# Kernel tuning notes

Measured on AMD Instinct MI355X. Metric: run time of the kernel, lower is better.

## Reference

```python
import jax, jax.numpy as jnp
import numpy as np

EPS = 1e-07


def unfold(a, p):
    # torch F.unfold(a, p, padding=(p-1)//2, stride=1): [B,C,H,W] -> [B, C*p*p, H*W]
    B, C, H, W = a.shape
    pad = (p - 1) // 2
    ap = jnp.pad(a, ((0, 0), (0, 0), (pad, pad), (pad, pad)))
    # channel ordering is C-major then (kh, kw), matching torch unfold
    patches = jnp.stack([ap[:, :, i:i + H, j:j + W] for i in range(p) for j in range(p)], axis=2)
    return patches.reshape(B, C * p * p, H * W)


def linear_attn(q, k, x):
    # q:[B,h,l1,d1]  k:[B,h,l2,d1]  x:[B,h,l2,d2]
    l1, d1 = q.shape[-2:]
    l2, d2 = x.shape[-2:]
    kt = jnp.swapaxes(k, -2, -1)  # [B,h,d1,l2]
    if l1 * d1 * l2 + l1 * l2 * d2 <= d2 * l2 * d1 + d2 * d1 * l1:
        s = q @ kt                                        # [B,h,l1,l2]
        s = s / (s.sum(axis=-1, keepdims=True) + EPS)
        return s @ x
    else:
        out = q @ (kt @ x)                                # [B,h,l1,d2]
        denom = q @ kt.sum(axis=-1, keepdims=True) + EPS  # [B,h,l1,1]
        return out / denom


def setup_inputs() -> dict:
    key = jax.random.key(0)
    k1, k2, k3, k4, k5 = jax.random.split(key, 5)
    B, C, H, W = 4, 64, 128, 128
    x = jax.random.normal(k1, (B, C, H, W), dtype=jnp.float32)
    qkv_w = jax.random.normal(k2, (3 * C, C), dtype=jnp.float32) * 0.05
    qkv_b = jax.random.normal(k3, (3 * C,), dtype=jnp.float32) * 0.01
    proj_w = jax.random.normal(k4, (C, C, 3, 3), dtype=jnp.float32) * 0.05
    proj_b = jax.random.normal(k5, (C,), dtype=jnp.float32) * 0.01
    return {"x": x, "qkv_w": qkv_w, "qkv_b": qkv_b, "proj_w": proj_w, "proj_b": proj_b}


def reference(x, qkv_w, qkv_b, proj_w, proj_b):
    numHeads, patchSize = 8, 3
    B, C, H, W = x.shape
    L = H * W
    # 1x1 conv qkv
    qkv = jnp.einsum('bchw,oc->bohw', x, qkv_w) + qkv_b[None, :, None, None]
    q, k, v = qkv[:, :C], qkv[:, C:2 * C], qkv[:, 2 * C:]
    q = jax.nn.relu(q)
    k = jax.nn.relu(k)
    q = unfold(q, patchSize)  # [B, C*p*p, L]
    k = unfold(k, patchSize)
    v = v.reshape(B, C, L)
    d1 = C * patchSize * patchSize
    assert d1 % numHeads == 0  # chosen so replicate-pad branch is skipped
    q = jnp.swapaxes(q.reshape(B, numHeads, d1 // numHeads, L), -1, -2)   # [B,h,L,d1h]
    k = jnp.swapaxes(k.reshape(B, numHeads, d1 // numHeads, L), -1, -2)
    v = jnp.swapaxes(v.reshape(B, numHeads, C // numHeads, L), -1, -2)    # [B,h,L,d2h]
    out = linear_attn(q, k, v)                                            # [B,h,L,d2h]
    out = jnp.swapaxes(out, -1, -2).reshape(B, C, H, W)
    # 3x3 conv proj, padding 1
    out = jax.lax.conv_general_dilated(out, proj_w, window_strides=(1, 1), padding='SAME',
                                       dimension_numbers=('NCHW', 'OIHW', 'NCHW'))
    out = out + proj_b[None, :, None, None]
    return out
```

## Files before the change

### kernel.cpp

```cpp
#include <hip/hip_runtime.h>
#include <hip/hip_fp16.h>

#define LL 16384
#define HH 128
#define WW 128
#define CC 64
#define NH 8
#define EPSF 1e-7f
#define KVCHUNKS 32

typedef __attribute__((ext_vector_type(8))) _Float16 f16x8;
typedef __attribute__((ext_vector_type(4))) float f32x4;
typedef __attribute__((ext_vector_type(8))) unsigned short u16x8;

static __device__ __forceinline__ unsigned short f2h_bits(float v) {
    const _Float16 h = (_Float16)v;
    unsigned short b;
    __builtin_memcpy(&b, &h, 2);
    return b;
}
static __device__ __forceinline__ float h2f_u16(unsigned short s) {
    _Float16 h;
    __builtin_memcpy(&h, &s, 2);
    return (float)h;
}
static __device__ __forceinline__ float h2f_lo(unsigned int u) {
    return h2f_u16((unsigned short)(u & 0xffffu));
}
static __device__ __forceinline__ float h2f_hi(unsigned int u) {
    return h2f_u16((unsigned short)(u >> 16));
}

__global__ void qkv_kernel(const float* __restrict__ x, const float* __restrict__ w,
                           const float* __restrict__ bias,
                           unsigned short* __restrict__ q, unsigned short* __restrict__ k,
                           unsigned short* __restrict__ v) {
    const int pix0 = blockIdx.x * 128;
    const int b    = blockIdx.y;
    const int sec  = blockIdx.z;
    const int tid  = threadIdx.x;
    const int lane = tid & 63;
    const int wv   = tid >> 6;

    __shared__ _Float16 xh[128][72], xl[128][72];
    __shared__ _Float16 wh[64][72],  wl[64][72];

    {
        const float* xb = x + (size_t)b * CC * LL + pix0;
        for (int idx = tid; idx < 64 * 128; idx += 256) {
            const int ci = idx >> 7;
            const int px = idx & 127;
            const float vv = xb[(size_t)ci * LL + px];
            const _Float16 h = (_Float16)vv;
            xh[px][ci] = h;
            xl[px][ci] = (_Float16)(vv - (float)h);
        }
    }
    {
        const float* wsec = w + (size_t)sec * 64 * 64;
        for (int idx = tid; idx < 64 * 64; idx += 256) {
            const int co = idx >> 6;
            const int ci = idx & 63;
            const float vv = wsec[co * 64 + ci];
            const _Float16 h = (_Float16)vv;
            wh[co][ci] = h;
            wl[co][ci] = (_Float16)(vv - (float)h);
        }
    }
    __syncthreads();

    f32x4 acc[4][2];
#pragma unroll
    for (int ct = 0; ct < 4; ++ct)
#pragma unroll
        for (int pt = 0; pt < 2; ++pt) acc[ct][pt] = (f32x4)0.f;

    const int g8 = (lane >> 4) * 8;
    const int rl = lane & 15;

#pragma unroll
    for (int ks = 0; ks < 2; ++ks) {
        const int kb = ks * 32 + g8;
        f16x8 ah[4], al[4], bh[2], bl[2];
#pragma unroll
        for (int ct = 0; ct < 4; ++ct) {
            ah[ct] = *(const f16x8*)&wh[ct * 16 + rl][kb];
            al[ct] = *(const f16x8*)&wl[ct * 16 + rl][kb];
        }
#pragma unroll
        for (int pt = 0; pt < 2; ++pt) {
            bh[pt] = *(const f16x8*)&xh[wv * 32 + pt * 16 + rl][kb];
            bl[pt] = *(const f16x8*)&xl[wv * 32 + pt * 16 + rl][kb];
        }
#pragma unroll
        for (int ct = 0; ct < 4; ++ct)
#pragma unroll
            for (int pt = 0; pt < 2; ++pt) {
                acc[ct][pt] = __builtin_amdgcn_mfma_f32_16x16x32_f16(ah[ct], bh[pt], acc[ct][pt], 0, 0, 0);
                acc[ct][pt] = __builtin_amdgcn_mfma_f32_16x16x32_f16(ah[ct], bl[pt], acc[ct][pt], 0, 0, 0);
                acc[ct][pt] = __builtin_amdgcn_mfma_f32_16x16x32_f16(al[ct], bh[pt], acc[ct][pt], 0, 0, 0);
            }
    }

    unsigned short* dst = (sec == 0) ? q : (sec == 1) ? k : v;
    const bool do_relu = (sec < 2);
#pragma unroll
    for (int ct = 0; ct < 4; ++ct) {
        const int co_b = ct * 16 + (lane >> 4) * 4;
#pragma unroll
        for (int pt = 0; pt < 2; ++pt) {
            const int px = pix0 + wv * 32 + pt * 16 + rl;
#pragma unroll
            for (int j = 0; j < 4; ++j) {
                const int co = co_b + j;
                float val = acc[ct][pt][j] + bias[sec * 64 + co];
                if (do_relu) val = fmaxf(val, 0.f);
                dst[((size_t)b * 64 + co) * LL + px] = f2h_bits(val);
            }
        }
    }
}

__global__ void kv_kernel(const unsigned short* __restrict__ k,
                          const unsigned short* __restrict__ v,
                          float* __restrict__ KVp) {
    const int chunk = blockIdx.x;
    const int h = blockIdx.y;
    const int b = blockIdx.z;
    const int tid = threadIdx.x;
    const int c  = tid >> 5;
    const int s  = tid & 31;
    const int half = s >> 4;
    const int sl   = s & 15;
    const int cpb  = half * 4;

    __shared__ float klds[8][6][130];

    {
        const unsigned short* kb = k + ((size_t)(b * 64) + 8 * h) * LL;
        for (int t = tid; t < 8 * 6 * 130; t += 256) {
            const int ch = t / 780;
            const int r1 = t - ch * 780;
            const int lr = r1 / 130;
            const int cx = r1 - lr * 130;
            const int gy = chunk * 4 + lr - 1;
            const int gx = cx - 1;
            const bool ok = (gy >= 0 && gy < HH && gx >= 0 && gx < WW);
            klds[ch][lr][cx] = ok ? h2f_u16(kb[(size_t)ch * LL + gy * WW + gx]) : 0.f;
        }
    }
    __syncthreads();

    const unsigned short* vb = v + ((size_t)(b * 64) + 8 * h + cpb) * LL;

    float kv4[9][4] = {{0.f}};
    float ks[9] = {0.f};

    for (int r = 0; r < 4; ++r) {
        const int y = chunk * 4 + r;
        for (int g = 0; g < 8; ++g) {
            const int col = g * 16 + sl;
            float vv[4];
#pragma unroll
            for (int cp = 0; cp < 4; ++cp) vv[cp] = h2f_u16(vb[(size_t)cp * LL + y * WW + col]);
            float k9[9];
#pragma unroll
            for (int dy = 0; dy < 3; ++dy)
#pragma unroll
                for (int dx = 0; dx < 3; ++dx)
                    k9[dy * 3 + dx] = klds[c][r + dy][col + dx];
#pragma unroll
            for (int p = 0; p < 9; ++p) {
                ks[p] += k9[p];
#pragma unroll
                for (int cp = 0; cp < 4; ++cp)
                    kv4[p][cp] = fmaf(k9[p], vv[cp], kv4[p][cp]);
            }
        }
    }

#pragma unroll
    for (int p = 0; p < 9; ++p) {
#pragma unroll
        for (int m = 8; m >= 1; m >>= 1) ks[p] += __shfl_xor(ks[p], m);
#pragma unroll
        for (int cp = 0; cp < 4; ++cp) {
#pragma unroll
            for (int m = 8; m >= 1; m >>= 1) kv4[p][cp] += __shfl_xor(kv4[p][cp], m);
        }
    }

    if (sl == 0) {
        float* dst = KVp + (((size_t)(b * NH + h) * KVCHUNKS) + chunk) * 648;
#pragma unroll
        for (int p = 0; p < 9; ++p) {
#pragma unroll
            for (int cp = 0; cp < 4; ++cp)
                dst[(c * 9 + p) * 8 + cpb + cp] = kv4[p][cp];
            if (half == 0) dst[576 + c * 9 + p] = ks[p];
        }
    }
}

__global__ void kv_finalize(const float* __restrict__ KVp,
                            float* __restrict__ KV, float* __restrict__ KS) {
    const int bh = blockIdx.x;
    const float* src = KVp + (size_t)bh * KVCHUNKS * 648;
    for (int idx = threadIdx.x; idx < 648; idx += 256) {
        float s0 = 0.f, s1 = 0.f, s2 = 0.f, s3 = 0.f;
#pragma unroll
        for (int ch = 0; ch < KVCHUNKS; ch += 4) {
            s0 += src[(ch + 0) * 648 + idx];
            s1 += src[(ch + 1) * 648 + idx];
            s2 += src[(ch + 2) * 648 + idx];
            s3 += src[(ch + 3) * 648 + idx];
        }
        const float sum = (s0 + s1) + (s2 + s3);
        if (idx < 576) KV[(size_t)bh * 576 + idx] = sum;
        else           KS[(size_t)bh * 72 + (idx - 576)] = sum;
    }
}

__global__ void attn_kernel(const unsigned short* __restrict__ q, const float* __restrict__ KV,
                            const float* __restrict__ KS, unsigned int* __restrict__ aofu) {
    const int y = blockIdx.x;
    const int h = blockIdx.y;
    const int b = blockIdx.z;
    const int t = threadIdx.x;

    float out0[8] = {0.f}, out1[8] = {0.f};
    float den0 = 0.f, den1 = 0.f;
    const int kvbase = (b * NH + h) * 8;
    const bool tlo = (t > 0), thi = (t < 63);

    for (int c = 0; c < 8; ++c) {
        const unsigned short* qc = q + ((size_t)(b * 64) + 8 * h + c) * LL;
        float qw[3][6];
#pragma unroll
        for (int dy = 0; dy < 3; ++dy) {
            const int yy = y + dy - 1;
            const bool yok = (yy >= 0 && yy < HH);
            const unsigned short* row = qc + yy * WW;
            const unsigned int u0 = (yok && tlo) ? *(const unsigned int*)(row + 2 * t - 2) : 0u;
            const unsigned int u1 = yok ? *(const unsigned int*)(row + 2 * t) : 0u;
            const unsigned int u2 = (yok && thi) ? *(const unsigned int*)(row + 2 * t + 2) : 0u;
            qw[dy][0] = h2f_lo(u0);  qw[dy][1] = h2f_hi(u0);
            qw[dy][2] = h2f_lo(u1);  qw[dy][3] = h2f_hi(u1);
            qw[dy][4] = h2f_lo(u2);  qw[dy][5] = h2f_hi(u2);
        }
        const float* kvr = KV + ((size_t)(kvbase + c) * 9) * 8;
        const float* ksr = KS + (size_t)(kvbase + c) * 9;
#pragma unroll
        for (int dy = 0; dy < 3; ++dy)
#pragma unroll
            for (int dx = 0; dx < 3; ++dx) {
                const int p = dy * 3 + dx;
                const float q0 = qw[dy][1 + dx];
                const float q1 = qw[dy][2 + dx];
                const float ksv = ksr[p];
                den0 = fmaf(q0, ksv, den0);
                den1 = fmaf(q1, ksv, den1);
#pragma unroll
                for (int cp = 0; cp < 8; ++cp) {
                    const float kvv = kvr[p * 8 + cp];
                    out0[cp] = fmaf(q0, kvv, out0[cp]);
                    out1[cp] = fmaf(q1, kvv, out1[cp]);
                }
            }
    }
    const float inv0 = 1.f / (den0 + EPSF);
    const float inv1 = 1.f / (den1 + EPSF);
    const int pixu = y * (WW / 2) + t;
#pragma unroll
    for (int cp = 0; cp < 8; ++cp) {
        const unsigned int lo = f2h_bits(out0[cp] * inv0);
        const unsigned int hi = f2h_bits(out1[cp] * inv1);
        aofu[((size_t)(b * 64) + h * 8 + cp) * (LL / 2) + pixu] = lo | (hi << 16);
    }
}

__global__ void wprep_kernel(const float* __restrict__ w, unsigned short* __restrict__ wfrag) {
    const int idx = blockIdx.x * 256 + threadIdx.x;
    const int k  = idx & 63;
    const int co = (idx >> 6) & 63;
    const int ks = idx >> 12;
    const int kg = ks * 64 + k;
    const int ci = kg >> 4, tap = kg & 15;
    const float vv = (tap < 9) ? w[(co * 64 + ci) * 9 + tap] : 0.f;
    const int kx = (((k >> 3) ^ (co & 7)) << 3) | (k & 7);
    wfrag[((size_t)ks * 64 + co) * 64 + kx] = f2h_bits(vv);
}

#define CONV_PREFETCH(KS)                                                        \
    do {                                                                         \
        const unsigned short* src_ = aofb + (size_t)((KS) * 4 + scis) * LL;      \
        pf0 = (oky0 && okxm) ? src_[offm - WW] : (unsigned short)0;              \
        pf1 = oky0 ? src_[off0 - WW] : (unsigned short)0;                        \
        pf2 = (oky0 && okxp) ? src_[offp - WW] : (unsigned short)0;              \
        pf3 = okxm ? src_[offm] : (unsigned short)0;                             \
        pf4 = src_[off0];                                                        \
        pf5 = okxp ? src_[offp] : (unsigned short)0;                             \
        pf6 = (oky2 && okxm) ? src_[offm + WW] : (unsigned short)0;              \
        pf7 = oky2 ? src_[off0 + WW] : (unsigned short)0;                        \
        pf8 = (oky2 && okxp) ? src_[offp + WW] : (unsigned short)0;              \
        const uint4* wsrc_ = (const uint4*)(wfrag + (size_t)(KS) * 4096);        \
        wf0 = wsrc_[tid];                                                        \
        wf1 = wsrc_[256 + tid];                                                  \
    } while (0)

__global__ __launch_bounds__(256) void conv_kernel(const unsigned short* __restrict__ aof,
                                                   const unsigned short* __restrict__ wfrag,
                                                   const float* __restrict__ bias,
                                                   float* __restrict__ out) {
    const int bid = blockIdx.x;
    const int swz = (bid & 7) * 128 + (bid >> 3);
    const int b = swz >> 8;
    const int rem = swz & 255;
    const int y = rem >> 1;
    const int colbase = (rem & 1) * 64;
    const int tid = threadIdx.x;
    const int lane = tid & 63;
    const int wv = tid >> 6;
    const int rl = lane & 15;
    const int g  = lane >> 4;

    __shared__ unsigned short plds[2][64 * 64];
    __shared__ unsigned short wlds[2][64 * 64];

    f32x4 acc[4];
#pragma unroll
    for (int ct = 0; ct < 4; ++ct) acc[ct] = (f32x4)0.f;

    const int spix = tid & 63;
    const int scis = tid >> 6;

    const unsigned short* aofb = aof + (size_t)b * 64 * LL;
    const int xc   = colbase + spix;
    const int off0 = y * WW + xc;
    const int offm = off0 - 1;
    const int offp = off0 + 1;
    const bool oky0 = (y > 0);
    const bool oky2 = (y < HH - 1);
    const bool okxm = (xc > 0);
    const bool okxp = (xc < WW - 1);
    const int xs0 = (((2 * scis)     ^ (spix & 7)) << 3);
    const int xs1 = (((2 * scis + 1) ^ (spix & 7)) << 3);

    unsigned short pf0, pf1, pf2, pf3, pf4, pf5, pf6, pf7, pf8;
    uint4 wf0, wf1;

    CONV_PREFETCH(0);

    for (int ks = 0; ks < 16; ++ks) {
        const int cur = ks & 1;
        {
            unsigned short h16[16];
            h16[0] = pf0;  h16[1] = pf1;  h16[2] = pf2;
            h16[3] = pf3;  h16[4] = pf4;  h16[5] = pf5;
            h16[6] = pf6;  h16[7] = pf7;  h16[8] = pf8;
#pragma unroll
            for (int j = 9; j < 16; ++j) h16[j] = 0;
            *(u16x8*)&plds[cur][spix * 64 + xs0] = *(u16x8*)&h16[0];
            *(u16x8*)&plds[cur][spix * 64 + xs1] = *(u16x8*)&h16[8];
            uint4* wdst = (uint4*)&wlds[cur][0];
            wdst[tid]       = wf0;
            wdst[256 + tid] = wf1;
        }
        __syncthreads();
        if (ks < 15) CONV_PREFETCH(ks + 1);

#pragma unroll
        for (int ksub = 0; ksub < 2; ++ksub) {
            const int xs = (((ksub * 4 + g) ^ (rl & 7)) << 3);
            const int row = wv * 16 + rl;
            const f16x8 bh = *(const f16x8*)&plds[cur][row * 64 + xs];
#pragma unroll
            for (int ct = 0; ct < 4; ++ct) {
                const int rowa = ct * 16 + rl;
                const f16x8 ah = *(const f16x8*)&wlds[cur][rowa * 64 + xs];
                acc[ct] = __builtin_amdgcn_mfma_f32_16x16x32_f16(ah, bh, acc[ct], 0, 0, 0);
            }
        }
    }

#pragma unroll
    for (int ct = 0; ct < 4; ++ct) {
        const int co_b = ct * 16 + g * 4;
        const int px = colbase + wv * 16 + rl;
#pragma unroll
        for (int j = 0; j < 4; ++j) {
            const int co = co_b + j;
            out[((size_t)b * 64 + co) * LL + y * WW + px] = acc[ct][j] + bias[co];
        }
    }
}

extern "C" void kernel_launch(void* const* d_in, const int* in_sizes, int n_in,
                              void* d_out, int out_size, void* d_ws, size_t ws_size,
                              hipStream_t stream) {
    const float* x      = (const float*)d_in[0];
    const float* qkv_w  = (const float*)d_in[1];
    const float* qkv_b  = (const float*)d_in[2];
    const float* proj_w = (const float*)d_in[3];
    const float* proj_b = (const float*)d_in[4];
    float* out = (float*)d_out;
    float* ws  = (float*)d_ws;

    const size_t n1 = (size_t)4 * 64 * LL;
    unsigned short* qb  = (unsigned short*)ws;
    unsigned short* kb  = (unsigned short*)(ws + n1);
    unsigned short* vb  = (unsigned short*)(ws + 2 * n1);
    unsigned short* aof = (unsigned short*)(ws + 3 * n1);
    float* KV   = ws + 4 * n1;
    float* KS   = KV + 4 * 8 * 8 * 9 * 8;
    float* KVp  = KS + 4 * 8 * 8 * 9;
    unsigned short* wfrag = (unsigned short*)(KVp + (size_t)32 * KVCHUNKS * 648);

    wprep_kernel<<<256, 256, 0, stream>>>(proj_w, wfrag);
    qkv_kernel<<<dim3(128, 4, 3), 256, 0, stream>>>(x, qkv_w, qkv_b, qb, kb, vb);
    kv_kernel<<<dim3(KVCHUNKS, NH, 4), 256, 0, stream>>>(kb, vb, KVp);
    kv_finalize<<<32, 256, 0, stream>>>(KVp, KV, KS);
    attn_kernel<<<dim3(128, NH, 4), 64, 0, stream>>>(qb, KV, KS, (unsigned int*)aof);
    conv_kernel<<<1024, 256, 0, stream>>>(aof, wfrag, proj_b, out);
}
```

Baseline: 103.3 us.

## Loop qkv sections in-block, stage outputs in LDS, vectorize kv loads

The qkv kernel now handles all three q/k/v sections in one block. It loads and splits x once instead of three times, then stages each section's fp16 output in shared memory so it can be written to global memory with coalesced 16-byte stores instead of scattered 2-byte stores. The kv kernel reads two adjacent fp16 v values per 32-bit load and processes two columns per iteration to cut load instructions. The trade-off is a 3x smaller qkv grid (512 blocks) with more barriers per block, which may lower parallelism.

```diff
diff --git a/kernel.cpp b/kernel.cpp
--- a/kernel.cpp
+++ b/kernel.cpp
@@ -37,13 +37,15 @@
                            unsigned short* __restrict__ v) {
     const int pix0 = blockIdx.x * 128;
     const int b    = blockIdx.y;
-    const int sec  = blockIdx.z;
     const int tid  = threadIdx.x;
     const int lane = tid & 63;
     const int wv   = tid >> 6;
 
     __shared__ _Float16 xh[128][72], xl[128][72];
-    __shared__ _Float16 wh[64][72],  wl[64][72];
+    __shared__ unsigned short wspace[2 * 64 * 72];
+    _Float16* whp = (_Float16*)wspace;
+    _Float16* wlp = whp + 64 * 72;
+    unsigned short* rep = wspace;
 
     {
         const float* xb = x + (size_t)b * CC * LL + pix0;
@@ -56,67 +58,81 @@
             xl[px][ci] = (_Float16)(vv - (float)h);
         }
     }
-    {
-        const float* wsec = w + (size_t)sec * 64 * 64;
-        for (int idx = tid; idx < 64 * 64; idx += 256) {
-            const int co = idx >> 6;
-            const int ci = idx & 63;
-            const float vv = wsec[co * 64 + ci];
-            const _Float16 h = (_Float16)vv;
-            wh[co][ci] = h;
-            wl[co][ci] = (_Float16)(vv - (float)h);
-        }
-    }
-    __syncthreads();
-
-    f32x4 acc[4][2];
-#pragma unroll
-    for (int ct = 0; ct < 4; ++ct)
-#pragma unroll
-        for (int pt = 0; pt < 2; ++pt) acc[ct][pt] = (f32x4)0.f;
 
     const int g8 = (lane >> 4) * 8;
     const int rl = lane & 15;
 
-#pragma unroll
-    for (int ks = 0; ks < 2; ++ks) {
-        const int kb = ks * 32 + g8;
-        f16x8 ah[4], al[4], bh[2], bl[2];
+    for (int sec = 0; sec < 3; ++sec) {
+        __syncthreads();
+        {
+            const float* wsec = w + (size_t)sec * 64 * 64;
+            for (int idx = tid; idx < 64 * 64; idx += 256) {
+                const int co = idx >> 6;
+                const int ci = idx & 63;
+                const float vv = wsec[co * 64 + ci];
+                const _Float16 h = (_Float16)vv;
+                whp[co * 72 + ci] = h;
+                wlp[co * 72 + ci] = (_Float16)(vv - (float)h);
+            }
+        }
+        __syncthreads();
+
+        f32x4 acc[4][2];
+#pragma unroll
+        for (int ct = 0; ct < 4; ++ct)
+#pragma unroll
+            for (int pt = 0; pt < 2; ++pt) acc[ct][pt] = (f32x4)0.f;
+
+#pragma unroll
+        for (int ks = 0; ks < 2; ++ks) {
+            const int kb = ks * 32 + g8;
+            f16x8 ah[4], al[4], bh[2], bl[2];
+#pragma unroll
+            for (int ct = 0; ct < 4; ++ct) {
+                ah[ct] = *(const f16x8*)&whp[(ct * 16 + rl) * 72 + kb];
+                al[ct] = *(const f16x8*)&wlp[(ct * 16 + rl) * 72 + kb];
+            }
+#pragma unroll
+            for (int pt = 0; pt < 2; ++pt) {
+                bh[pt] = *(const f16x8*)&xh[wv * 32 + pt * 16 + rl][kb];
+                bl[pt] = *(const f16x8*)&xl[wv * 32 + pt * 16 + rl][kb];
+            }
+#pragma unroll
+            for (int ct = 0; ct < 4; ++ct)
+#pragma unroll
+                for (int pt = 0; pt < 2; ++pt) {
+                    acc[ct][pt] = __builtin_amdgcn_mfma_f32_16x16x32_f16(ah[ct], bh[pt], acc[ct][pt], 0, 0, 0);
+                    acc[ct][pt] = __builtin_amdgcn_mfma_f32_16x16x32_f16(ah[ct], bl[pt], acc[ct][pt], 0, 0, 0);
+                    acc[ct][pt] = __builtin_amdgcn_mfma_f32_16x16x32_f16(al[ct], bh[pt], acc[ct][pt], 0, 0, 0);
+                }
+        }
+        __syncthreads();
+
+        const bool do_relu = (sec < 2);
 #pragma unroll
         for (int ct = 0; ct < 4; ++ct) {
-            ah[ct] = *(const f16x8*)&wh[ct * 16 + rl][kb];
-            al[ct] = *(const f16x8*)&wl[ct * 16 + rl][kb];
-        }
-#pragma unroll
-        for (int pt = 0; pt < 2; ++pt) {
-            bh[pt] = *(const f16x8*)&xh[wv * 32 + pt * 16 + rl][kb];
-            bl[pt] = *(const f16x8*)&xl[wv * 32 + pt * 16 + rl][kb];
-        }
-#pragma unroll
-        for (int ct = 0; ct < 4; ++ct)
+            const int co_b = ct * 16 + (lane >> 4) * 4;
 #pragma unroll
             for (int pt = 0; pt < 2; ++pt) {
-                acc[ct][pt] = __builtin_amdgcn_mfma_f32_16x16x32_f16(ah[ct], bh[pt], acc[ct][pt], 0, 0, 0);
-                acc[ct][pt] = __builtin_amdgcn_mfma_f32_16x16x32_f16(ah[ct], bl[pt], acc[ct][pt], 0, 0, 0);
-                acc[ct][pt] = __builtin_amdgcn_mfma_f32_16x16x32_f16(al[ct], bh[pt], acc[ct][pt], 0, 0, 0);
-            }
-    }
-
-    unsigned short* dst = (sec == 0) ? q : (sec == 1) ? k : v;
-    const bool do_relu = (sec < 2);
-#pragma unroll
-    for (int ct = 0; ct < 4; ++ct) {
-        const int co_b = ct * 16 + (lane >> 4) * 4;
-#pragma unroll
-        for (int pt = 0; pt < 2; ++pt) {
-            const int px = pix0 + wv * 32 + pt * 16 + rl;
-#pragma unroll
-            for (int j = 0; j < 4; ++j) {
-                const int co = co_b + j;
-                float val = acc[ct][pt][j] + bias[sec * 64 + co];
-                if (do_relu) val = fmaxf(val, 0.f);
-                dst[((size_t)b * 64 + co) * LL + px] = f2h_bits(val);
-            }
+                const int pxl = wv * 32 + pt * 16 + rl;
+#pragma unroll
+                for (int j = 0; j < 4; ++j) {
+                    const int co = co_b + j;
+                    float val = acc[ct][pt][j] + bias[sec * 64 + co];
+                    if (do_relu) val = fmaxf(val, 0.f);
+                    rep[co * 128 + pxl] = f2h_bits(val);
+                }
+            }
+        }
+        __syncthreads();
+
+        unsigned short* dst = ((sec == 0) ? q : (sec == 1) ? k : v) + (size_t)b * 64 * LL;
+#pragma unroll
+        for (int i = 0; i < 4; ++i) {
+            const int slot = i * 256 + tid;
+            const int co = slot >> 4;
+            const int u4 = slot & 15;
+            *(uint4*)(dst + (size_t)co * LL + pix0 + u4 * 8) = *(const uint4*)&rep[co * 128 + u4 * 8];
         }
     }
 }
@@ -151,31 +167,40 @@
     }
     __syncthreads();
 
-    const unsigned short* vb = v + ((size_t)(b * 64) + 8 * h + cpb) * LL;
+    const unsigned short* vbase = v + ((size_t)(b * 64) + 8 * h + cpb) * LL;
 
     float kv4[9][4] = {{0.f}};
     float ks[9] = {0.f};
 
     for (int r = 0; r < 4; ++r) {
         const int y = chunk * 4 + r;
-        for (int g = 0; g < 8; ++g) {
-            const int col = g * 16 + sl;
-            float vv[4];
-#pragma unroll
-            for (int cp = 0; cp < 4; ++cp) vv[cp] = h2f_u16(vb[(size_t)cp * LL + y * WW + col]);
-            float k9[9];
+        for (int g = 0; g < 4; ++g) {
+            const int col0 = g * 32 + sl * 2;
+            float va[4], vb2[4];
+#pragma unroll
+            for (int cp = 0; cp < 4; ++cp) {
+                const unsigned int u = *(const unsigned int*)(vbase + (size_t)cp * LL + y * WW + col0);
+                va[cp]  = h2f_lo(u);
+                vb2[cp] = h2f_hi(u);
+            }
+            float kw[3][4];
 #pragma unroll
             for (int dy = 0; dy < 3; ++dy)
 #pragma unroll
-                for (int dx = 0; dx < 3; ++dx)
-                    k9[dy * 3 + dx] = klds[c][r + dy][col + dx];
-#pragma unroll
-            for (int p = 0; p < 9; ++p) {
-                ks[p] += k9[p];
-#pragma unroll
-                for (int cp = 0; cp < 4; ++cp)
-                    kv4[p][cp] = fmaf(k9[p], vv[cp], kv4[p][cp]);
-            }
+                for (int dxx = 0; dxx < 4; ++dxx)
+                    kw[dy][dxx] = klds[c][r + dy][col0 + dxx];
+#pragma unroll
+            for (int dy = 0; dy < 3; ++dy)
+#pragma unroll
+                for (int dx = 0; dx < 3; ++dx) {
+                    const int p = dy * 3 + dx;
+                    const float ka  = kw[dy][dx];
+                    const float kb2 = kw[dy][dx + 1];
+                    ks[p] += ka + kb2;
+#pragma unroll
+                    for (int cp = 0; cp < 4; ++cp)
+                        kv4[p][cp] = fmaf(kb2, vb2[cp], fmaf(ka, va[cp], kv4[p][cp]));
+                }
         }
     }
 
@@ -417,7 +442,7 @@
     unsigned short* wfrag = (unsigned short*)(KVp + (size_t)32 * KVCHUNKS * 648);
 
     wprep_kernel<<<256, 256, 0, stream>>>(proj_w, wfrag);
-    qkv_kernel<<<dim3(128, 4, 3), 256, 0, stream>>>(x, qkv_w, qkv_b, qb, kb, vb);
+    qkv_kernel<<<dim3(128, 4), 256, 0, stream>>>(x, qkv_w, qkv_b, qb, kb, vb);
     kv_kernel<<<dim3(KVCHUNKS, NH, 4), 256, 0, stream>>>(kb, vb, KVp);
     kv_finalize<<<32, 256, 0, stream>>>(KVp, KV, KS);
     attn_kernel<<<dim3(128, NH, 4), 64, 0, stream>>>(qb, KV, KS, (unsigned int*)aof);
```

Measured after the change: 100.8 us. -2.4%, faster.
